# Kernel optimization log

Measured on AMD Instinct MI355X. Metric: run time of the kernel, lower is better.

Reference implementation:

```python
import jax, jax.numpy as jnp
import numpy as np

N_NODES = 100_000
N_EDGES = 800_000
IN_DIM = 128
OUT_DIM = 128
H = 8
D = OUT_DIM // H  # head dim = 16
SCALE = float(np.sqrt(OUT_DIM / H))


def setup_inputs() -> dict:
    key = jax.random.key(0)
    k1, k2, k3, k4, k5 = jax.random.split(key, 5)
    x = jax.random.normal(k1, (N_NODES, IN_DIM), dtype=jnp.float32)
    i_node = jax.random.randint(k2, (N_EDGES,), 0, N_NODES)
    j_node = jax.random.randint(k3, (N_EDGES,), 0, N_NODES)
    # nn.Linear weights (bias=False): [out_features, in_features]
    Wqkv = jax.random.normal(k4, (3 * OUT_DIM, IN_DIM), dtype=jnp.float32) / np.sqrt(IN_DIM)
    Wprj = jax.random.normal(k5, (OUT_DIM, OUT_DIM), dtype=jnp.float32) / np.sqrt(OUT_DIM)
    return {"x": x, "Wqkv": Wqkv, "Wprj": Wprj, "i_node": i_node, "j_node": j_node}


def reference(x, Wqkv, Wprj, i_node, j_node):
    N = x.shape[0]
    # node_tf_qkv then einops 'n (h d3) -> h n d3'; we keep [N, H, 3D] layout
    qkv = (x @ Wqkv.T).reshape(N, H, 3 * D)
    q, k, v = qkv[..., :D], qkv[..., D:2 * D], qkv[..., 2 * D:]  # chunk(dim=-1)
    q_e = q[i_node]   # [E, H, D] gather target-node queries
    k_e = k[j_node]   # [E, H, D] gather source-node keys
    v_e = v[j_node]   # [E, H, D] gather source-node values
    alpha = (q_e * k_e).sum(-1) / SCALE          # [E, H] per-edge scores
    # segment softmax grouped by target node i_node (torch_geometric softmax)
    m = jax.ops.segment_max(alpha, i_node, num_segments=N)      # [N, H]
    m = jnp.where(jnp.isfinite(m), m, 0.0)                      # nodes with no edges
    ex = jnp.exp(alpha - m[i_node])                             # [E, H]
    denom = jax.ops.segment_sum(ex, i_node, num_segments=N)     # [N, H]
    w = ex / (denom[i_node] + 1e-16)                            # [E, H]
    # scatter-add weighted values back to target nodes
    out = jax.ops.segment_sum(v_e * w[..., None], i_node, num_segments=N)  # [N, H, D]
    out = out.reshape(N, H * D)                  # einops 'h n d -> n (h d)'
    return out @ Wprj.T
```

## Files before the change

kernel.cpp:

```cpp
#include <hip/hip_runtime.h>
#include <hip/hip_bf16.h>
#include <math.h>

#define N_NODES 100000
#define N_EDGES 800000
#define CAP     64

typedef __bf16 bf16x8 __attribute__((ext_vector_type(8)));
typedef float  f32x4  __attribute__((ext_vector_type(4)));

__device__ inline unsigned short f2bf(float f) {
    unsigned u = __float_as_uint(f);
    u += 0x7FFF + ((u >> 16) & 1);
    return (unsigned short)(u >> 16);
}
__device__ inline float bflo(unsigned u) { return __uint_as_float(u << 16); }
__device__ inline float bfhi(unsigned u) { return __uint_as_float(u & 0xFFFF0000u); }
__device__ inline float2 bfpair(unsigned u) { return make_float2(bflo(u), bfhi(u)); }

__global__ __launch_bounds__(256) void cvt_wqkv_perm(
    const float* __restrict__ in, unsigned short* __restrict__ out)
{
    int idx = blockIdx.x * 256 + threadIdx.x;
    if (idx >= 12288) return;
    int r = idx >> 5, c4 = idx & 31;
    int h = r / 48, rem = r - h * 48;
    int part = rem >> 4, d = rem & 15;
    int nr = part * 128 + h * 16 + d;
    float4 v = ((const float4*)in)[idx];
    ushort4 o;
    o.x = f2bf(v.x); o.y = f2bf(v.y); o.z = f2bf(v.z); o.w = f2bf(v.w);
    ((ushort4*)out)[(nr << 5) + c4] = o;
}

__global__ __launch_bounds__(256) void cvt_bf16(
    const float* __restrict__ in, unsigned short* __restrict__ out, int n4)
{
    int i = blockIdx.x * 256 + threadIdx.x;
    if (i >= n4) return;
    float4 v = ((const float4*)in)[i];
    ushort4 o;
    o.x = f2bf(v.x); o.y = f2bf(v.y); o.z = f2bf(v.z); o.w = f2bf(v.w);
    ((ushort4*)out)[i] = o;
}

template<bool AFP32, bool BF16OUT>
__global__ __launch_bounds__(256) void gemm_mfma(
    const void* __restrict__ Av, int M,
    const unsigned short* __restrict__ B,
    void* __restrict__ C, int Nb)
{
    __shared__ unsigned short As[64][136];
    __shared__ unsigned short Bs[64][136];
    const int t = threadIdx.x;
    const int row0 = blockIdx.x * 64;

    #pragma unroll
    for (int u = 0; u < 4; ++u) {
        int idx = t + u * 256;
        int r = idx >> 4, c = idx & 15;
        int gr = row0 + r;
        if (AFP32) {
            const float* ap = (const float*)Av + (size_t)gr * 128 + c * 8;
            float4 a0 = make_float4(0.f, 0.f, 0.f, 0.f), a1 = a0;
            if (gr < M) { a0 = ((const float4*)ap)[0]; a1 = ((const float4*)ap)[1]; }
            unsigned w0 = (unsigned)f2bf(a0.x) | ((unsigned)f2bf(a0.y) << 16);
            unsigned w1 = (unsigned)f2bf(a0.z) | ((unsigned)f2bf(a0.w) << 16);
            unsigned w2 = (unsigned)f2bf(a1.x) | ((unsigned)f2bf(a1.y) << 16);
            unsigned w3 = (unsigned)f2bf(a1.z) | ((unsigned)f2bf(a1.w) << 16);
            *(uint4*)&As[r][c * 8] = make_uint4(w0, w1, w2, w3);
        } else {
            float4 val = make_float4(0.f, 0.f, 0.f, 0.f);
            if (gr < M)
                val = *(const float4*)((const unsigned short*)Av + (size_t)gr * 128 + c * 8);
            *(float4*)&As[r][c * 8] = val;
        }
    }

    const int wid = t >> 6, lane = t & 63;
    const int wm = wid >> 1, wn = wid & 1;
    const int lrow = lane & 15, kg = lane >> 4;

    for (int ct = 0; ct < Nb / 64; ++ct) {
        #pragma unroll
        for (int u = 0; u < 4; ++u) {
            int idx = t + u * 256;
            int r = idx >> 4, c = idx & 15;
            float4 val = *(const float4*)(B + (size_t)(ct * 64 + r) * 128 + c * 8);
            *(float4*)&Bs[r][c * 8] = val;
        }
        __syncthreads();

        f32x4 acc[2][2] = {};
        #pragma unroll
        for (int ks = 0; ks < 4; ++ks) {
            bf16x8 af[2], bfr[2];
            #pragma unroll
            for (int m = 0; m < 2; ++m)
                af[m] = *(const bf16x8*)&As[wm * 32 + m * 16 + lrow][ks * 32 + kg * 8];
            #pragma unroll
            for (int n = 0; n < 2; ++n)
                bfr[n] = *(const bf16x8*)&Bs[wn * 32 + n * 16 + lrow][ks * 32 + kg * 8];
            #pragma unroll
            for (int m = 0; m < 2; ++m)
                #pragma unroll
                for (int n = 0; n < 2; ++n)
                    acc[m][n] = __builtin_amdgcn_mfma_f32_16x16x32_bf16(
                        af[m], bfr[n], acc[m][n], 0, 0, 0);
        }

        #pragma unroll
        for (int m = 0; m < 2; ++m)
            #pragma unroll
            for (int reg = 0; reg < 4; ++reg) {
                int gr = row0 + wm * 32 + m * 16 + kg * 4 + reg;
                if (gr < M) {
                    #pragma unroll
                    for (int n = 0; n < 2; ++n) {
                        int gc = ct * 64 + wn * 32 + n * 16 + lrow;
                        if (BF16OUT)
                            ((unsigned short*)C)[(size_t)gr * Nb + gc] = f2bf(acc[m][n][reg]);
                        else
                            ((float*)C)[(size_t)gr * Nb + gc] = acc[m][n][reg];
                    }
                }
            }
        __syncthreads();
    }
}

__global__ __launch_bounds__(256) void scatter_cap(
    const int* __restrict__ i_node, const int* __restrict__ j_node,
    unsigned* __restrict__ cnt, int* __restrict__ jlist)
{
    int e = blockIdx.x * 256 + threadIdx.x;
    if (e < N_EDGES) {
        int i = i_node[e];
        unsigned pos = atomicAdd(&cnt[i], 1u);
        jlist[(size_t)i * CAP + pos] = j_node[e] * 384;
    }
}

__global__ __launch_bounds__(256) void node_gather(
    const unsigned short* __restrict__ qkv,
    const unsigned* __restrict__ cnt,
    const int* __restrict__ jlist,
    unsigned short* __restrict__ accum)
{
    int n = blockIdx.x * 4 + (threadIdx.x >> 6);
    if (n >= N_NODES) return;
    int lane = threadIdx.x & 63;
    int slot = lane >> 3, h = lane & 7;

    const uint4* qp = (const uint4*)(qkv + (size_t)n * 384 + h * 16);
    uint4 q0 = qp[0], q1 = qp[1];
    float2 qf[8];
    qf[0] = bfpair(q0.x); qf[1] = bfpair(q0.y); qf[2] = bfpair(q0.z); qf[3] = bfpair(q0.w);
    qf[4] = bfpair(q1.x); qf[5] = bfpair(q1.y); qf[6] = bfpair(q1.z); qf[7] = bfpair(q1.w);

    unsigned deg = cnt[n];
    const int* jrow = jlist + (size_t)n * CAP;

    float2 acc[8] = {};
    float dsum = 0.f;
    for (unsigned it = 0; it < deg; it += 8) {
        unsigned idx = it + (unsigned)slot;
        bool act = idx < deg;
        int jb = jrow[act ? idx : 0];
        const uint4* kp = (const uint4*)(qkv + (size_t)jb + 128 + h * 16);
        uint4 k0 = kp[0], k1 = kp[1];
        uint4 v0 = kp[16], v1 = kp[17];
        float2 kf[8], vf[8];
        kf[0] = bfpair(k0.x); kf[1] = bfpair(k0.y); kf[2] = bfpair(k0.z); kf[3] = bfpair(k0.w);
        kf[4] = bfpair(k1.x); kf[5] = bfpair(k1.y); kf[6] = bfpair(k1.z); kf[7] = bfpair(k1.w);
        vf[0] = bfpair(v0.x); vf[1] = bfpair(v0.y); vf[2] = bfpair(v0.z); vf[3] = bfpair(v0.w);
        vf[4] = bfpair(v1.x); vf[5] = bfpair(v1.y); vf[6] = bfpair(v1.z); vf[7] = bfpair(v1.w);
        float2 d2 = make_float2(0.f, 0.f);
        #pragma unroll
        for (int i = 0; i < 8; ++i) d2 += qf[i] * kf[i];
        float ex = act ? __expf((d2.x + d2.y) * 0.25f) : 0.f;
        dsum += ex;
        float2 ex2 = make_float2(ex, ex);
        #pragma unroll
        for (int i = 0; i < 8; ++i) acc[i] += vf[i] * ex2;
    }

    float* accf = (float*)acc;
    #pragma unroll
    for (int off = 8; off < 64; off <<= 1) {
        dsum += __shfl_xor(dsum, off);
        #pragma unroll
        for (int i = 0; i < 16; ++i) accf[i] += __shfl_xor(accf[i], off);
    }

    if (slot == 0) {
        float rs = 1.0f / (dsum + 1e-16f);
        unsigned o[8];
        #pragma unroll
        for (int i = 0; i < 8; ++i)
            o[i] = (unsigned)f2bf(acc[i].x * rs)
                 | ((unsigned)f2bf(acc[i].y * rs) << 16);
        uint4* ap = (uint4*)(accum + (size_t)n * 128 + h * 16);
        ap[0] = make_uint4(o[0], o[1], o[2], o[3]);
        ap[1] = make_uint4(o[4], o[5], o[6], o[7]);
    }
}

extern "C" void kernel_launch(void* const* d_in, const int* in_sizes, int n_in,
                              void* d_out, int out_size, void* d_ws, size_t ws_size,
                              hipStream_t stream) {
    const float* x      = (const float*)d_in[0];
    const float* Wqkv   = (const float*)d_in[1];
    const float* Wprj   = (const float*)d_in[2];
    const int*   i_node = (const int*)d_in[3];
    const int*   j_node = (const int*)d_in[4];
    float* out = (float*)d_out;

    char* w = (char*)d_ws;
    unsigned short* qkvbf  = (unsigned short*)w;  w += (size_t)N_NODES * 384 * 2;
    unsigned short* accbf  = (unsigned short*)w;  w += (size_t)N_NODES * 128 * 2;
    unsigned short* wqkvbf = (unsigned short*)w;  w += 384 * 128 * 2;
    unsigned short* wprjbf = (unsigned short*)w;  w += 128 * 128 * 2;
    unsigned* cnt = (unsigned*)w;  w += N_NODES * 4;
    int* jlist = (int*)w;

    hipMemsetAsync(cnt, 0, N_NODES * sizeof(unsigned), stream);

    cvt_wqkv_perm<<<48, 256, 0, stream>>>(Wqkv, wqkvbf);
    cvt_bf16<<<16, 256, 0, stream>>>(Wprj, wprjbf, 4096);

    scatter_cap<<<(N_EDGES + 255) / 256, 256, 0, stream>>>(i_node, j_node, cnt, jlist);

    gemm_mfma<true, true><<<(N_NODES + 63) / 64, 256, 0, stream>>>(
        x, N_NODES, wqkvbf, qkvbf, 384);

    node_gather<<<(N_NODES + 3) / 4, 256, 0, stream>>>(qkvbf, cnt, jlist, accbf);

    gemm_mfma<false, false><<<(N_NODES + 63) / 64, 256, 0, stream>>>(
        accbf, N_NODES, wprjbf, out, 128);
}
```

Baseline: 264.6 us.

## Remap node_gather lanes, prefetch GEMM B tiles, merge weight conversion kernels

In node_gather, a head's 16 dims are now split across two lanes, with 16 lanes per edge and 4 edges processed at once instead of 8. The dot product is finished with a shuffle, and each K/V load becomes one contiguous 16-byte load per lane. The GEMM now prefetches the next B tile into registers while the current tile is computed, and the trailing barrier moves to the top of the loop. The two weight-conversion kernels are merged into one launch. The gather trades fewer registers and better coalescing for more loop iterations per node.

```diff
diff --git a/kernel.cpp b/kernel.cpp
--- a/kernel.cpp
+++ b/kernel.cpp
@@ -18,30 +18,27 @@
 __device__ inline float bfhi(unsigned u) { return __uint_as_float(u & 0xFFFF0000u); }
 __device__ inline float2 bfpair(unsigned u) { return make_float2(bflo(u), bfhi(u)); }
 
-__global__ __launch_bounds__(256) void cvt_wqkv_perm(
-    const float* __restrict__ in, unsigned short* __restrict__ out)
+__global__ __launch_bounds__(256) void cvt_weights(
+    const float* __restrict__ wqkv, const float* __restrict__ wprj,
+    unsigned short* __restrict__ wqkvbf, unsigned short* __restrict__ wprjbf)
 {
     int idx = blockIdx.x * 256 + threadIdx.x;
-    if (idx >= 12288) return;
-    int r = idx >> 5, c4 = idx & 31;
-    int h = r / 48, rem = r - h * 48;
-    int part = rem >> 4, d = rem & 15;
-    int nr = part * 128 + h * 16 + d;
-    float4 v = ((const float4*)in)[idx];
-    ushort4 o;
-    o.x = f2bf(v.x); o.y = f2bf(v.y); o.z = f2bf(v.z); o.w = f2bf(v.w);
-    ((ushort4*)out)[(nr << 5) + c4] = o;
-}
-
-__global__ __launch_bounds__(256) void cvt_bf16(
-    const float* __restrict__ in, unsigned short* __restrict__ out, int n4)
-{
-    int i = blockIdx.x * 256 + threadIdx.x;
-    if (i >= n4) return;
-    float4 v = ((const float4*)in)[i];
-    ushort4 o;
-    o.x = f2bf(v.x); o.y = f2bf(v.y); o.z = f2bf(v.z); o.w = f2bf(v.w);
-    ((ushort4*)out)[i] = o;
+    if (idx < 12288) {
+        int r = idx >> 5, c4 = idx & 31;
+        int h = r / 48, rem = r - h * 48;
+        int part = rem >> 4, d = rem & 15;
+        int nr = part * 128 + h * 16 + d;
+        float4 v = ((const float4*)wqkv)[idx];
+        ushort4 o;
+        o.x = f2bf(v.x); o.y = f2bf(v.y); o.z = f2bf(v.z); o.w = f2bf(v.w);
+        ((ushort4*)wqkvbf)[(nr << 5) + c4] = o;
+    } else {
+        int i = idx - 12288;
+        float4 v = ((const float4*)wprj)[i];
+        ushort4 o;
+        o.x = f2bf(v.x); o.y = f2bf(v.y); o.z = f2bf(v.z); o.w = f2bf(v.w);
+        ((ushort4*)wprjbf)[i] = o;
+    }
 }
 
 template<bool AFP32, bool BF16OUT>
@@ -80,14 +77,23 @@
     const int wid = t >> 6, lane = t & 63;
     const int wm = wid >> 1, wn = wid & 1;
     const int lrow = lane & 15, kg = lane >> 4;
-
-    for (int ct = 0; ct < Nb / 64; ++ct) {
-        #pragma unroll
-        for (int u = 0; u < 4; ++u) {
-            int idx = t + u * 256;
-            int r = idx >> 4, c = idx & 15;
-            float4 val = *(const float4*)(B + (size_t)(ct * 64 + r) * 128 + c * 8);
-            *(float4*)&Bs[r][c * 8] = val;
+    const int br = t >> 4, bc = (t & 15) * 8;
+
+    float4 pb[4];
+    #pragma unroll
+    for (int u = 0; u < 4; ++u)
+        pb[u] = *(const float4*)(B + (size_t)(br + u * 16) * 128 + bc);
+
+    const int NT = Nb / 64;
+    for (int ct = 0; ct < NT; ++ct) {
+        __syncthreads();
+        #pragma unroll
+        for (int u = 0; u < 4; ++u)
+            *(float4*)&Bs[br + u * 16][bc] = pb[u];
+        if (ct + 1 < NT) {
+            #pragma unroll
+            for (int u = 0; u < 4; ++u)
+                pb[u] = *(const float4*)(B + (size_t)((ct + 1) * 64 + br + u * 16) * 128 + bc);
         }
         __syncthreads();
 
@@ -125,7 +131,6 @@
                     }
                 }
             }
-        __syncthreads();
     }
 }
 
@@ -150,59 +155,51 @@
     int n = blockIdx.x * 4 + (threadIdx.x >> 6);
     if (n >= N_NODES) return;
     int lane = threadIdx.x & 63;
-    int slot = lane >> 3, h = lane & 7;
-
-    const uint4* qp = (const uint4*)(qkv + (size_t)n * 384 + h * 16);
-    uint4 q0 = qp[0], q1 = qp[1];
-    float2 qf[8];
-    qf[0] = bfpair(q0.x); qf[1] = bfpair(q0.y); qf[2] = bfpair(q0.z); qf[3] = bfpair(q0.w);
-    qf[4] = bfpair(q1.x); qf[5] = bfpair(q1.y); qf[6] = bfpair(q1.z); qf[7] = bfpair(q1.w);
+    int slot = lane >> 4, r = lane & 15;
+
+    const uint4 q = *(const uint4*)(qkv + (size_t)n * 384 + r * 8);
+    float2 qf[4] = { bfpair(q.x), bfpair(q.y), bfpair(q.z), bfpair(q.w) };
 
     unsigned deg = cnt[n];
     const int* jrow = jlist + (size_t)n * CAP;
 
-    float2 acc[8] = {};
+    float2 acc[4] = {};
     float dsum = 0.f;
-    for (unsigned it = 0; it < deg; it += 8) {
+    for (unsigned it = 0; it < deg; it += 4) {
         unsigned idx = it + (unsigned)slot;
         bool act = idx < deg;
         int jb = jrow[act ? idx : 0];
-        const uint4* kp = (const uint4*)(qkv + (size_t)jb + 128 + h * 16);
-        uint4 k0 = kp[0], k1 = kp[1];
-        uint4 v0 = kp[16], v1 = kp[17];
-        float2 kf[8], vf[8];
-        kf[0] = bfpair(k0.x); kf[1] = bfpair(k0.y); kf[2] = bfpair(k0.z); kf[3] = bfpair(k0.w);
-        kf[4] = bfpair(k1.x); kf[5] = bfpair(k1.y); kf[6] = bfpair(k1.z); kf[7] = bfpair(k1.w);
-        vf[0] = bfpair(v0.x); vf[1] = bfpair(v0.y); vf[2] = bfpair(v0.z); vf[3] = bfpair(v0.w);
-        vf[4] = bfpair(v1.x); vf[5] = bfpair(v1.y); vf[6] = bfpair(v1.z); vf[7] = bfpair(v1.w);
-        float2 d2 = make_float2(0.f, 0.f);
-        #pragma unroll
-        for (int i = 0; i < 8; ++i) d2 += qf[i] * kf[i];
-        float ex = act ? __expf((d2.x + d2.y) * 0.25f) : 0.f;
+        const unsigned short* kb = qkv + (size_t)jb + 128 + r * 8;
+        uint4 kq = *(const uint4*)kb;
+        uint4 vq = *(const uint4*)(kb + 128);
+        float2 kf0 = bfpair(kq.x), kf1 = bfpair(kq.y), kf2 = bfpair(kq.z), kf3 = bfpair(kq.w);
+        float2 d2 = qf[0] * kf0 + qf[1] * kf1 + qf[2] * kf2 + qf[3] * kf3;
+        float ah = d2.x + d2.y;
+        ah += __shfl_xor(ah, 1);
+        float ex = act ? __expf(ah * 0.25f) : 0.f;
         dsum += ex;
-        float2 ex2 = make_float2(ex, ex);
-        #pragma unroll
-        for (int i = 0; i < 8; ++i) acc[i] += vf[i] * ex2;
-    }
-
-    float* accf = (float*)acc;
+        float2 e2 = make_float2(ex, ex);
+        acc[0] += bfpair(vq.x) * e2;
+        acc[1] += bfpair(vq.y) * e2;
+        acc[2] += bfpair(vq.z) * e2;
+        acc[3] += bfpair(vq.w) * e2;
+    }
+
+    float* af = (float*)acc;
     #pragma unroll
-    for (int off = 8; off < 64; off <<= 1) {
+    for (int off = 16; off < 64; off <<= 1) {
         dsum += __shfl_xor(dsum, off);
         #pragma unroll
-        for (int i = 0; i < 16; ++i) accf[i] += __shfl_xor(accf[i], off);
+        for (int i = 0; i < 8; ++i) af[i] += __shfl_xor(af[i], off);
     }
 
     if (slot == 0) {
         float rs = 1.0f / (dsum + 1e-16f);
-        unsigned o[8];
-        #pragma unroll
-        for (int i = 0; i < 8; ++i)
-            o[i] = (unsigned)f2bf(acc[i].x * rs)
-                 | ((unsigned)f2bf(acc[i].y * rs) << 16);
-        uint4* ap = (uint4*)(accum + (size_t)n * 128 + h * 16);
-        ap[0] = make_uint4(o[0], o[1], o[2], o[3]);
-        ap[1] = make_uint4(o[4], o[5], o[6], o[7]);
+        unsigned o0 = (unsigned)f2bf(acc[0].x * rs) | ((unsigned)f2bf(acc[0].y * rs) << 16);
+        unsigned o1 = (unsigned)f2bf(acc[1].x * rs) | ((unsigned)f2bf(acc[1].y * rs) << 16);
+        unsigned o2 = (unsigned)f2bf(acc[2].x * rs) | ((unsigned)f2bf(acc[2].y * rs) << 16);
+        unsigned o3 = (unsigned)f2bf(acc[3].x * rs) | ((unsigned)f2bf(acc[3].y * rs) << 16);
+        *(uint4*)(accum + (size_t)n * 128 + r * 8) = make_uint4(o0, o1, o2, o3);
     }
 }
 
@@ -226,8 +223,7 @@
 
     hipMemsetAsync(cnt, 0, N_NODES * sizeof(unsigned), stream);
 
-    cvt_wqkv_perm<<<48, 256, 0, stream>>>(Wqkv, wqkvbf);
-    cvt_bf16<<<16, 256, 0, stream>>>(Wprj, wprjbf, 4096);
+    cvt_weights<<<64, 256, 0, stream>>>(Wqkv, Wprj, wqkvbf, wprjbf);
 
     scatter_cap<<<(N_EDGES + 255) / 256, 256, 0, stream>>>(i_node, j_node, cnt, jlist);
 
```

Measured after the change: 315.0 us. 19.1% more time.
